# Performance work log

Measured on AMD Instinct MI355X. Metric: run time of the kernel, lower is better.

## Reference

```python
import jax, jax.numpy as jnp
import numpy as np

NEAR = 0.01          # near-plane clip for camera-space depth
BLUR = 0.3           # 2D covariance dilation used by 3DGS/gsplat rasterizers
MAX_ALPHA = 0.999    # alpha clamp used by 3DGS/gsplat


def _quat_to_rotmat(q):
    # q: [N,4] normalized (w, x, y, z)
    w, x, y, z = q[:, 0], q[:, 1], q[:, 2], q[:, 3]
    return jnp.stack([
        jnp.stack([1 - 2 * (y * y + z * z), 2 * (x * y - w * z), 2 * (x * z + w * y)], -1),
        jnp.stack([2 * (x * y + w * z), 1 - 2 * (x * x + z * z), 2 * (y * z - w * x)], -1),
        jnp.stack([2 * (x * z - w * y), 2 * (y * z + w * x), 1 - 2 * (x * x + y * y)], -1),
    ], -2)  # [N,3,3]


def _render_one(viewmat, K, means, quats_n, scales, opacities, colors, width, height):
    # --- 3D covariance: Sigma = R diag(s^2) R^T ---
    R = _quat_to_rotmat(quats_n)                      # [N,3,3]
    M = R * scales[:, None, :]                        # scale columns
    cov3d = jnp.einsum('nij,nkj->nik', M, M)          # [N,3,3]

    # --- project means to camera / image ---
    Rcw, tvec = viewmat[:3, :3], viewmat[:3, 3]
    tc = means @ Rcw.T + tvec                         # [N,3] camera-space
    tz = tc[:, 2]
    fx, fy, cx, cy = K[0, 0], K[1, 1], K[0, 2], K[1, 2]
    tz_safe = jnp.where(tz > NEAR, tz, NEAR)
    inv_z = 1.0 / tz_safe
    mean2d = jnp.stack([fx * tc[:, 0] * inv_z + cx,
                        fy * tc[:, 1] * inv_z + cy], -1)  # [N,2]

    # --- EWA splatting: cov2d = J W Sigma W^T J^T + blur*I ---
    zeros = jnp.zeros_like(inv_z)
    J = jnp.stack([
        jnp.stack([fx * inv_z, zeros, -fx * tc[:, 0] * inv_z * inv_z], -1),
        jnp.stack([zeros, fy * inv_z, -fy * tc[:, 1] * inv_z * inv_z], -1),
    ], -2)                                            # [N,2,3]
    cov_cam = jnp.einsum('ij,njk,lk->nil', Rcw, cov3d, Rcw)
    cov2d = jnp.einsum('nij,njk,nlk->nil', J, cov_cam, J)
    a = cov2d[:, 0, 0] + BLUR
    c = cov2d[:, 1, 1] + BLUR
    b = cov2d[:, 0, 1]
    det = a * c - b * b
    valid = (tz > NEAR) & (det > 1e-12)
    det_s = jnp.where(valid, det, 1.0)
    ia, ib, ic = c / det_s, -b / det_s, a / det_s     # conic (inverse cov2d)

    # --- depth sort (front to back) ---
    order = jnp.argsort(tz)
    mean2d, ia, ib, ic = mean2d[order], ia[order], ib[order], ic[order]
    opac_s, colors_s, valid_s = opacities[order], colors[order], valid[order]

    # --- per-pixel gaussian evaluation (pixel centers at +0.5) ---
    px = jnp.arange(width, dtype=mean2d.dtype) + 0.5   # [W]
    py = jnp.arange(height, dtype=mean2d.dtype) + 0.5  # [H]
    dx = px[:, None] - mean2d[None, :, 0]              # [W,N]
    dy = py[:, None] - mean2d[None, :, 1]              # [H,N]
    quad = (ia * dx * dx)[None, :, :] \
         + 2.0 * ib * dx[None, :, :] * dy[:, None, :] \
         + (ic * dy * dy)[:, None, :]                  # [H,W,N]
    alpha = opac_s * jnp.exp(-0.5 * quad)
    alpha = jnp.where(valid_s, jnp.minimum(alpha, MAX_ALPHA), 0.0)

    # --- front-to-back alpha compositing ---
    Tinc = jnp.cumprod(1.0 - alpha, axis=-1)
    Texc = jnp.concatenate([jnp.ones_like(Tinc[..., :1]), Tinc[..., :-1]], -1)
    w = alpha * Texc                                   # [H,W,N]
    return jnp.einsum('hwn,nc->hwc', w, colors_s)      # [H,W,3]


def reference(viewmats, Ks, means, quats, log_scales, opacity_logits, color_logits, width, height):
    # parameter activations (GaussianSplat.activated_parameters)
    quats_n = quats / jnp.linalg.norm(quats, axis=-1, keepdims=True)
    scales = jnp.exp(log_scales)
    opac = jax.nn.sigmoid(opacity_logits)
    colors = jax.nn.sigmoid(color_logits)
    render = lambda vm, K: _render_one(vm, K, means, quats_n, scales, opac, colors, width, height)
    return jax.vmap(render)(viewmats, Ks)  # [C,H,W,3]


def setup_inputs() -> dict:
    key = jax.random.key(0)
    k1, k2, k3 = jax.random.split(key, 3)
    N = 1024
    means = jax.random.normal(k1, (N, 3), dtype=jnp.float32) * 0.1
    quats = jnp.concatenate([jnp.ones((N, 1), jnp.float32),
                             jnp.zeros((N, 3), jnp.float32)], -1)
    quats = quats + 0.1 * jax.random.normal(k3, (N, 4), dtype=jnp.float32)
    log_scales = jnp.full((N, 3), -2.3, dtype=jnp.float32)
    opacity_logits = jnp.full((N,), -1.0, dtype=jnp.float32)
    color_logits = jax.random.normal(k2, (N, 3), dtype=jnp.float32)

    def look(angle):
        c, s = np.cos(angle), np.sin(angle)
        vm = np.eye(4, dtype=np.float32)
        vm[:3, :3] = np.array([[c, 0, -s], [0, 1, 0], [s, 0, c]], np.float32)
        vm[:3, 3] = np.array([0, 0, 2.5], np.float32)
        return vm

    viewmats = jnp.asarray(np.stack([look(0.0), look(0.4)]))
    K = np.array([[128.0, 0, 64.0], [0, 128.0, 64.0], [0, 0, 1.0]], np.float32)
    Ks = jnp.asarray(np.stack([K, K]))
    return {"viewmats": viewmats, "Ks": Ks, "means": means, "quats": quats,
            "log_scales": log_scales, "opacity_logits": opacity_logits,
            "color_logits": color_logits, "width": 128, "height": 128}
```

## Files before the change

kernel.cpp:

```cpp
#include <hip/hip_runtime.h>
#include <math.h>

#define NEARP 0.01f
#define BLUR 0.3f
#define MAX_ALPHA 0.999f
#define TILE 16
#define NSEG 8
#define SEGMAX 256

__device__ __forceinline__ float sigmoidf_(float x) {
    return 1.0f / (1.0f + expf(-x));
}

__global__ void gs_preprocess(const float* __restrict__ viewmats,
                              const float* __restrict__ Ks,
                              const float* __restrict__ means,
                              const float* __restrict__ quats,
                              const float* __restrict__ log_scales,
                              const float* __restrict__ opac_logits,
                              const float* __restrict__ color_logits,
                              float4* __restrict__ unsorted,
                              float* __restrict__ tz_out,
                              int N, int C) {
    int idx = blockIdx.x * blockDim.x + threadIdx.x;
    if (idx >= N * C) return;
    int c = idx / N;
    int n = idx - c * N;

    float qw = quats[n * 4 + 0], qx = quats[n * 4 + 1];
    float qy = quats[n * 4 + 2], qz = quats[n * 4 + 3];
    float qn = rsqrtf(qw * qw + qx * qx + qy * qy + qz * qz);
    float w = qw * qn, x = qx * qn, y = qy * qn, z = qz * qn;
    float R00 = 1.0f - 2.0f * (y * y + z * z), R01 = 2.0f * (x * y - w * z), R02 = 2.0f * (x * z + w * y);
    float R10 = 2.0f * (x * y + w * z), R11 = 1.0f - 2.0f * (x * x + z * z), R12 = 2.0f * (y * z - w * x);
    float R20 = 2.0f * (x * z - w * y), R21 = 2.0f * (y * z + w * x), R22 = 1.0f - 2.0f * (x * x + y * y);

    float s0 = expf(log_scales[n * 3 + 0]);
    float s1 = expf(log_scales[n * 3 + 1]);
    float s2 = expf(log_scales[n * 3 + 2]);

    float M00 = R00 * s0, M01 = R01 * s1, M02 = R02 * s2;
    float M10 = R10 * s0, M11 = R11 * s1, M12 = R12 * s2;
    float M20 = R20 * s0, M21 = R21 * s1, M22 = R22 * s2;
    float C00 = M00 * M00 + M01 * M01 + M02 * M02;
    float C01 = M00 * M10 + M01 * M11 + M02 * M12;
    float C02 = M00 * M20 + M01 * M21 + M02 * M22;
    float C11 = M10 * M10 + M11 * M11 + M12 * M12;
    float C12 = M10 * M20 + M11 * M21 + M12 * M22;
    float C22 = M20 * M20 + M21 * M21 + M22 * M22;

    const float* vm = viewmats + c * 16;
    float V00 = vm[0], V01 = vm[1], V02 = vm[2], T0 = vm[3];
    float V10 = vm[4], V11 = vm[5], V12 = vm[6], T1 = vm[7];
    float V20 = vm[8], V21 = vm[9], V22 = vm[10], T2 = vm[11];
    float mex = means[n * 3 + 0], mey = means[n * 3 + 1], mez = means[n * 3 + 2];
    float tx = V00 * mex + V01 * mey + V02 * mez + T0;
    float ty = V10 * mex + V11 * mey + V12 * mez + T1;
    float tz = V20 * mex + V21 * mey + V22 * mez + T2;

    float fx = Ks[c * 9 + 0], fy = Ks[c * 9 + 4], cx = Ks[c * 9 + 2], cy = Ks[c * 9 + 5];
    float tzs = (tz > NEARP) ? tz : NEARP;
    float iz = 1.0f / tzs;
    float m2x = fx * tx * iz + cx;
    float m2y = fy * ty * iz + cy;

    float A00 = V00 * C00 + V01 * C01 + V02 * C02;
    float A01 = V00 * C01 + V01 * C11 + V02 * C12;
    float A02 = V00 * C02 + V01 * C12 + V02 * C22;
    float A10 = V10 * C00 + V11 * C01 + V12 * C02;
    float A11 = V10 * C01 + V11 * C11 + V12 * C12;
    float A12 = V10 * C02 + V11 * C12 + V12 * C22;
    float A20 = V20 * C00 + V21 * C01 + V22 * C02;
    float A21 = V20 * C01 + V21 * C11 + V22 * C12;
    float A22 = V20 * C02 + V21 * C12 + V22 * C22;
    float S00 = A00 * V00 + A01 * V01 + A02 * V02;
    float S01 = A00 * V10 + A01 * V11 + A02 * V12;
    float S02 = A00 * V20 + A01 * V21 + A02 * V22;
    float S11 = A10 * V10 + A11 * V11 + A12 * V12;
    float S12 = A10 * V20 + A11 * V21 + A12 * V22;
    float S22 = A20 * V20 + A21 * V21 + A22 * V22;

    float J00 = fx * iz, J02 = -fx * tx * iz * iz;
    float J11 = fy * iz, J12 = -fy * ty * iz * iz;

    float c2_00 = J00 * J00 * S00 + 2.0f * J00 * J02 * S02 + J02 * J02 * S22;
    float c2_01 = J00 * J11 * S01 + J00 * J12 * S02 + J02 * J11 * S12 + J02 * J12 * S22;
    float c2_11 = J11 * J11 * S11 + 2.0f * J11 * J12 * S12 + J12 * J12 * S22;

    float a = c2_00 + BLUR;
    float cc = c2_11 + BLUR;
    float b = c2_01;
    float det = a * cc - b * b;
    bool valid = (tz > NEARP) && (det > 1e-12f);

    float ia, ib, ic, op;
    if (valid) {
        float inv = 1.0f / det;
        ia = cc * inv;
        ib = -b * inv;
        ic = a * inv;
        op = sigmoidf_(opac_logits[n]);
    } else {
        ia = 0.0f; ib = 0.0f; ic = 0.0f; op = 0.0f;
    }
    float cr = sigmoidf_(color_logits[n * 3 + 0]);
    float cg = sigmoidf_(color_logits[n * 3 + 1]);
    float cb = sigmoidf_(color_logits[n * 3 + 2]);

    size_t base = (size_t)(c * N + n) * 3;
    unsorted[base + 0] = make_float4(m2x, m2y, ia, ib);
    unsorted[base + 1] = make_float4(ic, op, cr, cg);
    unsorted[base + 2] = make_float4(cb, 0.0f, 0.0f, 0.0f);
    tz_out[c * N + n] = tz;
}

__global__ void gs_sort_wave(const float4* __restrict__ unsorted,
                             const float* __restrict__ tzin,
                             float4* __restrict__ sorted,
                             int N, int C) {
    int gtid = blockIdx.x * blockDim.x + threadIdx.x;
    int wid = gtid >> 6;
    int lane = gtid & 63;
    if (wid >= C * N) return;
    int c = wid / N;
    int i = wid - c * N;
    const float* tzc = tzin + (size_t)c * N;
    float ti = tzc[i];
    int rank = 0;
    for (int j = lane; j < N; j += 64) {
        float tj = tzc[j];
        rank += (int)((tj < ti) || (tj == ti && j < i));
    }
#pragma unroll
    for (int off = 1; off < 64; off <<= 1)
        rank += __shfl_xor(rank, off, 64);
    size_t src = (size_t)(c * N + i) * 3;
    size_t dst = (size_t)(c * N + rank) * 3;
    if (lane < 3) sorted[dst + lane] = unsorted[src + lane];
}

__global__ void __launch_bounds__(256) gs_render_seg(const float4* __restrict__ sorted,
                                                     float4* __restrict__ partial,
                                                     int N, int W, int H,
                                                     int nseg, int seglen) {
    __shared__ float4 sg[SEGMAX * 3];
    int zc = blockIdx.z;
    int c = zc / nseg;
    int s = zc - c * nseg;
    int g0 = s * seglen;
    int g1 = min(N, g0 + seglen);

    int lx = threadIdx.x % TILE;
    int ly = threadIdx.x / TILE;
    int x = blockIdx.x * TILE + lx;
    int y = blockIdx.y * TILE + ly;
    float px = (float)x + 0.5f;
    float py = (float)y + 0.5f;

    float T = 1.0f, accr = 0.0f, accg = 0.0f, accb = 0.0f;
    const float4* base = sorted + (size_t)c * N * 3;

    for (int start = g0; start < g1; start += SEGMAX) {
        int cnt = min(SEGMAX, g1 - start);
        __syncthreads();
        for (int t = threadIdx.x; t < cnt * 3; t += blockDim.x)
            sg[t] = base[(size_t)start * 3 + t];
        __syncthreads();
        if (__any(T > 1e-6f)) {
#pragma unroll 4
            for (int k = 0; k < cnt; k++) {
                float4 f0 = sg[k * 3 + 0];
                float4 f1 = sg[k * 3 + 1];
                float4 f2 = sg[k * 3 + 2];
                float dx = px - f0.x;
                float dy = py - f0.y;
                float quad = f0.z * dx * dx + 2.0f * f0.w * dx * dy + f1.x * dy * dy;
                float alpha = f1.y * __expf(-0.5f * quad);
                alpha = fminf(alpha, MAX_ALPHA);
                float wgt = alpha * T;
                accr += wgt * f1.z;
                accg += wgt * f1.w;
                accb += wgt * f2.x;
                T *= (1.0f - alpha);
            }
        }
    }
    if (x < W && y < H) {
        partial[((size_t)zc * H + y) * W + x] = make_float4(accr, accg, accb, T);
    }
}

__global__ void gs_combine(const float4* __restrict__ partial,
                           float* __restrict__ out,
                           int W, int H, int nseg, int C) {
    int pid = blockIdx.x * blockDim.x + threadIdx.x;
    int PIX = W * H;
    if (pid >= C * PIX) return;
    int c = pid / PIX;
    int p = pid - c * PIX;
    float T = 1.0f, r = 0.0f, g = 0.0f, b = 0.0f;
    for (int s = 0; s < nseg; s++) {
        float4 ps = partial[(size_t)(c * nseg + s) * PIX + p];
        r += T * ps.x;
        g += T * ps.y;
        b += T * ps.z;
        T *= ps.w;
    }
    size_t o = (size_t)pid * 3;
    out[o + 0] = r;
    out[o + 1] = g;
    out[o + 2] = b;
}

extern "C" void kernel_launch(void* const* d_in, const int* in_sizes, int n_in,
                              void* d_out, int out_size, void* d_ws, size_t ws_size,
                              hipStream_t stream) {
    const float* viewmats = (const float*)d_in[0];
    const float* Ks = (const float*)d_in[1];
    const float* means = (const float*)d_in[2];
    const float* quats = (const float*)d_in[3];
    const float* log_scales = (const float*)d_in[4];
    const float* opac_logits = (const float*)d_in[5];
    const float* color_logits = (const float*)d_in[6];
    float* out = (float*)d_out;

    int N = in_sizes[2] / 3;
    int C = in_sizes[0] / 16;
    int pix = out_size / (C * 3);
    int W = (int)(sqrt((double)pix) + 0.5);
    int H = pix / W;

    float4* sorted = (float4*)d_ws;
    float4* unsorted = sorted + (size_t)C * N * 3;
    float* tzbuf = (float*)(unsorted + (size_t)C * N * 3);
    float4* partial = (float4*)(tzbuf + (size_t)C * N);
    partial = (float4*)(((uintptr_t)partial + 15) & ~(uintptr_t)15);

    int total = C * N;
    gs_preprocess<<<(total + 255) / 256, 256, 0, stream>>>(
        viewmats, Ks, means, quats, log_scales, opac_logits, color_logits,
        unsorted, tzbuf, N, C);

    int sort_threads = total * 64;
    gs_sort_wave<<<(sort_threads + 255) / 256, 256, 0, stream>>>(
        unsorted, tzbuf, sorted, N, C);

    int nseg = NSEG;
    int seglen = (N + nseg - 1) / nseg;
    dim3 grid((W + TILE - 1) / TILE, (H + TILE - 1) / TILE, C * nseg);
    gs_render_seg<<<grid, 256, 0, stream>>>(sorted, partial, N, W, H, nseg, seglen);

    int cp = C * W * H;
    gs_combine<<<(cp + 255) / 256, 256, 0, stream>>>(partial, out, W, H, nseg, C);
}
```

Before: 102.1 us.

## Cull Gaussians per tile via bounding radius and render only tile lists

Preprocess now computes a screen-space radius from the largest eigenvalue of the 2D covariance, with a quadratic cutoff. A new kernel builds a per-tile list of overlapping depth-sorted Gaussians using wave ballots. The render kernel splits only that tile's list across 16 segments instead of all Gaussians over 8. The payload shrinks to two float4s: conic terms pre-scaled for exp2, and red/green packed as half2. This cuts wasted exp and blend work on tiles far from a Gaussian, at the cost of an extra kernel, indirect global loads in place of the shared-memory staging, the loss of the early-exit check, and small approximation from the cutoff and half-precision colours.

```diff
diff --git a/kernel.cpp b/kernel.cpp
--- a/kernel.cpp
+++ b/kernel.cpp
@@ -1,12 +1,13 @@
 #include <hip/hip_runtime.h>
+#include <hip/hip_fp16.h>
 #include <math.h>
 
 #define NEARP 0.01f
 #define BLUR 0.3f
 #define MAX_ALPHA 0.999f
 #define TILE 16
-#define NSEG 8
-#define SEGMAX 256
+#define NSEG 16
+#define QCUT 32.0f
 
 __device__ __forceinline__ float sigmoidf_(float x) {
     return 1.0f / (1.0f + expf(-x));
@@ -19,7 +20,8 @@
                               const float* __restrict__ log_scales,
                               const float* __restrict__ opac_logits,
                               const float* __restrict__ color_logits,
-                              float4* __restrict__ unsorted,
+                              float4* __restrict__ ubbox,
+                              float4* __restrict__ upay,
                               float* __restrict__ tz_out,
                               int N, int C) {
     int idx = blockIdx.x * blockDim.x + threadIdx.x;
@@ -93,30 +95,43 @@
     float det = a * cc - b * b;
     bool valid = (tz > NEARP) && (det > 1e-12f);
 
-    float ia, ib, ic, op;
+    float ia, ib, ic, op, r;
     if (valid) {
         float inv = 1.0f / det;
         ia = cc * inv;
         ib = -b * inv;
         ic = a * inv;
         op = sigmoidf_(opac_logits[n]);
+        float lmax = 0.5f * (a + cc) + sqrtf(0.25f * (a - cc) * (a - cc) + b * b);
+        r = sqrtf(QCUT * lmax);
     } else {
         ia = 0.0f; ib = 0.0f; ic = 0.0f; op = 0.0f;
+        r = -1.0f;
     }
     float cr = sigmoidf_(color_logits[n * 3 + 0]);
     float cg = sigmoidf_(color_logits[n * 3 + 1]);
     float cb = sigmoidf_(color_logits[n * 3 + 2]);
 
-    size_t base = (size_t)(c * N + n) * 3;
-    unsorted[base + 0] = make_float4(m2x, m2y, ia, ib);
-    unsorted[base + 1] = make_float4(ic, op, cr, cg);
-    unsorted[base + 2] = make_float4(cb, 0.0f, 0.0f, 0.0f);
-    tz_out[c * N + n] = tz;
-}
-
-__global__ void gs_sort_wave(const float4* __restrict__ unsorted,
+    const float KQ = 0.721347520444482f;
+    float iap = -KQ * ia;
+    float ibp = -2.0f * KQ * ib;
+    float icp = -KQ * ic;
+
+    union { __half2 h; float f; } pk;
+    pk.h = __floats2half2_rn(cr, cg);
+
+    int gi = c * N + n;
+    ubbox[gi] = make_float4(m2x, m2y, r, 0.0f);
+    upay[(size_t)gi * 2 + 0] = make_float4(m2x, m2y, iap, ibp);
+    upay[(size_t)gi * 2 + 1] = make_float4(icp, op, pk.f, cb);
+    tz_out[gi] = tz;
+}
+
+__global__ void gs_sort_wave(const float4* __restrict__ ubbox,
+                             const float4* __restrict__ upay,
                              const float* __restrict__ tzin,
-                             float4* __restrict__ sorted,
+                             float4* __restrict__ sbbox,
+                             float4* __restrict__ spay,
                              int N, int C) {
     int gtid = blockIdx.x * blockDim.x + threadIdx.x;
     int wid = gtid >> 6;
@@ -134,21 +149,67 @@
 #pragma unroll
     for (int off = 1; off < 64; off <<= 1)
         rank += __shfl_xor(rank, off, 64);
-    size_t src = (size_t)(c * N + i) * 3;
-    size_t dst = (size_t)(c * N + rank) * 3;
-    if (lane < 3) sorted[dst + lane] = unsorted[src + lane];
-}
-
-__global__ void __launch_bounds__(256) gs_render_seg(const float4* __restrict__ sorted,
-                                                     float4* __restrict__ partial,
-                                                     int N, int W, int H,
-                                                     int nseg, int seglen) {
-    __shared__ float4 sg[SEGMAX * 3];
+    int src = c * N + i;
+    int dst = c * N + rank;
+    if (lane == 0) sbbox[dst] = ubbox[src];
+    if (lane < 2) spay[(size_t)dst * 2 + lane] = upay[(size_t)src * 2 + lane];
+}
+
+__global__ void gs_tilebuild(const float4* __restrict__ sbbox,
+                             int* __restrict__ tcount,
+                             int* __restrict__ tlist,
+                             int N, int C, int tilesx, int tilesy) {
+    int gtid = blockIdx.x * blockDim.x + threadIdx.x;
+    int wid = gtid >> 6;
+    int lane = gtid & 63;
+    int T = tilesx * tilesy;
+    if (wid >= C * T) return;
+    int c = wid / T;
+    int t = wid - c * T;
+    float x0 = (float)((t % tilesx) * TILE);
+    float y0 = (float)((t / tilesx) * TILE);
+    float x1 = x0 + (float)TILE;
+    float y1 = y0 + (float)TILE;
+
+    const float4* bb = sbbox + (size_t)c * N;
+    int* lst = tlist + (size_t)wid * N;
+    int cnt = 0;
+    for (int base = 0; base < N; base += 64) {
+        int g = base + lane;
+        bool pred = false;
+        if (g < N) {
+            float4 b = bb[g];
+            pred = (b.z >= 0.0f) &&
+                   (b.x - b.z <= x1) && (b.x + b.z >= x0) &&
+                   (b.y - b.z <= y1) && (b.y + b.z >= y0);
+        }
+        unsigned long long bal = __ballot(pred);
+        if (pred) {
+            int off = __popcll(bal & ((1ull << lane) - 1ull));
+            lst[cnt + off] = g;
+        }
+        cnt += (int)__popcll(bal);
+    }
+    if (lane == 0) tcount[wid] = cnt;
+}
+
+__global__ void __launch_bounds__(256) gs_render_tile(const float4* __restrict__ spay,
+                                                      const int* __restrict__ tcount,
+                                                      const int* __restrict__ tlist,
+                                                      float4* __restrict__ partial,
+                                                      int N, int W, int H,
+                                                      int tilesx, int nseg) {
     int zc = blockIdx.z;
     int c = zc / nseg;
     int s = zc - c * nseg;
-    int g0 = s * seglen;
-    int g1 = min(N, g0 + seglen);
+    int t = blockIdx.y * tilesx + blockIdx.x;
+    int T = tilesx * ((H + TILE - 1) / TILE);
+    int wid = c * T + t;
+
+    int cnt = tcount[wid];
+    int L = (cnt + nseg - 1) / nseg;
+    int k0 = s * L;
+    int k1 = min(cnt, k0 + L);
 
     int lx = threadIdx.x % TILE;
     int ly = threadIdx.x / TILE;
@@ -157,36 +218,29 @@
     float px = (float)x + 0.5f;
     float py = (float)y + 0.5f;
 
-    float T = 1.0f, accr = 0.0f, accg = 0.0f, accb = 0.0f;
-    const float4* base = sorted + (size_t)c * N * 3;
-
-    for (int start = g0; start < g1; start += SEGMAX) {
-        int cnt = min(SEGMAX, g1 - start);
-        __syncthreads();
-        for (int t = threadIdx.x; t < cnt * 3; t += blockDim.x)
-            sg[t] = base[(size_t)start * 3 + t];
-        __syncthreads();
-        if (__any(T > 1e-6f)) {
+    float Tr = 1.0f, accr = 0.0f, accg = 0.0f, accb = 0.0f;
+    const int* lst = tlist + (size_t)wid * N;
+    const float4* pay = spay + (size_t)c * N * 2;
+
 #pragma unroll 4
-            for (int k = 0; k < cnt; k++) {
-                float4 f0 = sg[k * 3 + 0];
-                float4 f1 = sg[k * 3 + 1];
-                float4 f2 = sg[k * 3 + 2];
-                float dx = px - f0.x;
-                float dy = py - f0.y;
-                float quad = f0.z * dx * dx + 2.0f * f0.w * dx * dy + f1.x * dy * dy;
-                float alpha = f1.y * __expf(-0.5f * quad);
-                alpha = fminf(alpha, MAX_ALPHA);
-                float wgt = alpha * T;
-                accr += wgt * f1.z;
-                accg += wgt * f1.w;
-                accb += wgt * f2.x;
-                T *= (1.0f - alpha);
-            }
-        }
+    for (int k = k0; k < k1; k++) {
+        int idx = lst[k];
+        float4 f0 = pay[(size_t)idx * 2 + 0];
+        float4 f1 = pay[(size_t)idx * 2 + 1];
+        float dx = px - f0.x;
+        float dy = py - f0.y;
+        float quad = dx * (f0.z * dx + f0.w * dy) + f1.x * dy * dy;
+        float alpha = f1.y * exp2f(quad);
+        alpha = fminf(alpha, MAX_ALPHA);
+        union { float f; __half2 h; } pk; pk.f = f1.z;
+        float wgt = alpha * Tr;
+        accr += wgt * __low2float(pk.h);
+        accg += wgt * __high2float(pk.h);
+        accb += wgt * f1.w;
+        Tr *= (1.0f - alpha);
     }
     if (x < W && y < H) {
-        partial[((size_t)zc * H + y) * W + x] = make_float4(accr, accg, accb, T);
+        partial[((size_t)zc * H + y) * W + x] = make_float4(accr, accg, accb, Tr);
     }
 }
 
@@ -229,26 +283,34 @@
     int pix = out_size / (C * 3);
     int W = (int)(sqrt((double)pix) + 0.5);
     int H = pix / W;
-
-    float4* sorted = (float4*)d_ws;
-    float4* unsorted = sorted + (size_t)C * N * 3;
-    float* tzbuf = (float*)(unsorted + (size_t)C * N * 3);
-    float4* partial = (float4*)(tzbuf + (size_t)C * N);
-    partial = (float4*)(((uintptr_t)partial + 15) & ~(uintptr_t)15);
+    int tilesx = (W + TILE - 1) / TILE;
+    int tilesy = (H + TILE - 1) / TILE;
+    int T = tilesx * tilesy;
+    int nseg = NSEG;
+
+    float4* ubbox = (float4*)d_ws;
+    float4* sbbox = ubbox + (size_t)C * N;
+    float4* upay  = sbbox + (size_t)C * N;
+    float4* spay  = upay + (size_t)C * N * 2;
+    float4* partial = spay + (size_t)C * N * 2;
+    float*  tzbuf = (float*)(partial + (size_t)C * nseg * pix);
+    int*    tcount = (int*)(tzbuf + (size_t)C * N);
+    int*    tlist  = tcount + (size_t)C * T;
 
     int total = C * N;
     gs_preprocess<<<(total + 255) / 256, 256, 0, stream>>>(
         viewmats, Ks, means, quats, log_scales, opac_logits, color_logits,
-        unsorted, tzbuf, N, C);
-
-    int sort_threads = total * 64;
-    gs_sort_wave<<<(sort_threads + 255) / 256, 256, 0, stream>>>(
-        unsorted, tzbuf, sorted, N, C);
-
-    int nseg = NSEG;
-    int seglen = (N + nseg - 1) / nseg;
-    dim3 grid((W + TILE - 1) / TILE, (H + TILE - 1) / TILE, C * nseg);
-    gs_render_seg<<<grid, 256, 0, stream>>>(sorted, partial, N, W, H, nseg, seglen);
+        ubbox, upay, tzbuf, N, C);
+
+    gs_sort_wave<<<(total * 64 + 255) / 256, 256, 0, stream>>>(
+        ubbox, upay, tzbuf, sbbox, spay, N, C);
+
+    gs_tilebuild<<<(C * T * 64 + 255) / 256, 256, 0, stream>>>(
+        sbbox, tcount, tlist, N, C, tilesx, tilesy);
+
+    dim3 grid(tilesx, tilesy, C * nseg);
+    gs_render_tile<<<grid, 256, 0, stream>>>(
+        spay, tcount, tlist, partial, N, W, H, tilesx, nseg);
 
     int cp = C * W * H;
     gs_combine<<<(cp + 255) / 256, 256, 0, stream>>>(partial, out, W, H, nseg, C);
```

After: 114.4 us. 12.1% more time.
